# Optimization experiments

Hardware: AMD Instinct MI355X
Metric: run time of the kernel (lower is better)

Reference implementation:

```python
import jax, jax.numpy as jnp
import numpy as np

B, NV, NQ = 32, 512, 128
V_DIM, Q_DIM, H_DIM, K, H_OUT = 2048, 1024, 512, 3, 8
HK = H_DIM * K  # 1536


def setup_inputs() -> dict:
    key = jax.random.key(0)
    ks = jax.random.split(key, 8)
    s_v = 1.0 / np.sqrt(V_DIM)
    s_q = 1.0 / np.sqrt(Q_DIM)
    return {
        "v": jax.random.normal(ks[0], (B, NV, V_DIM), dtype=jnp.float32),
        "q": jax.random.normal(ks[1], (B, NQ, Q_DIM), dtype=jnp.float32),
        "Wv": jax.random.uniform(ks[2], (HK, V_DIM), jnp.float32, -s_v, s_v),
        "bv": jax.random.uniform(ks[3], (HK,), jnp.float32, -s_v, s_v),
        "Wq": jax.random.uniform(ks[4], (HK, Q_DIM), jnp.float32, -s_q, s_q),
        "bq": jax.random.uniform(ks[5], (HK,), jnp.float32, -s_q, s_q),
        "h_mat": jax.random.normal(ks[6], (H_OUT, HK), dtype=jnp.float32),
        "h_bias": jax.random.normal(ks[7], (H_OUT,), dtype=jnp.float32),
    }


def reference(v, q, Wv, bv, Wq, bq, h_mat, h_bias):
    # FCNet (single weight-norm Linear + ReLU); dropout is identity at eval.
    v_ = jax.nn.relu(jnp.einsum('bvd,kd->bvk', v, Wv) + bv)  # (B, NV, HK)
    q_ = jax.nn.relu(jnp.einsum('bqd,kd->bqk', q, Wq) + bq)  # (B, NQ, HK)
    # Three-way low-rank bilinear contraction over the rank dim k.
    logits = jnp.einsum('hk,bvk,bqk->bhvq', h_mat, v_, q_)
    return logits + h_bias[None, :, None, None]
```

## Files before the change

kernel.cpp:

```cpp
#include <hip/hip_runtime.h>


typedef _Float16 h8 __attribute__((ext_vector_type(8)));
typedef float f32x4 __attribute__((ext_vector_type(4)));

#define B_   32
#define NV_  512
#define NQ_  128
#define VD_  2048
#define QD_  1024
#define HK_  1536
#define HO_  8

__device__ __forceinline__ void gload_lds16(const void* g, void* l) {
  __builtin_amdgcn_global_load_lds(
      (const __attribute__((address_space(1))) void*)g,
      (__attribute__((address_space(3))) void*)l, 16, 0, 0);
}

__global__ __launch_bounds__(256) void cvt_all(
    const float* __restrict__ v, const float* __restrict__ q,
    const float* __restrict__ Wv, const float* __restrict__ Wq,
    const float* __restrict__ hm,
    _Float16* __restrict__ v16, _Float16* __restrict__ q16,
    _Float16* __restrict__ Wv16, _Float16* __restrict__ Wq16,
    _Float16* __restrict__ h16) {
  int i = blockIdx.x * blockDim.x + threadIdx.x;
  const float* src;
  _Float16* dst;
  if (i < 4194304)      { src = v;  dst = v16; }
  else if (i < 4718592) { src = q;  dst = q16;  i -= 4194304; }
  else if (i < 5111808) { src = Wv; dst = Wv16; i -= 4718592; }
  else if (i < 5308416) { src = Wq; dst = Wq16; i -= 5111808; }
  else                  { src = hm; dst = h16;  i -= 5308416; }
  const float4* p = (const float4*)src;
  float4 a = p[i * 2], b = p[i * 2 + 1];
  h8 o;
  o[0] = (_Float16)a.x; o[1] = (_Float16)a.y; o[2] = (_Float16)a.z; o[3] = (_Float16)a.w;
  o[4] = (_Float16)b.x; o[5] = (_Float16)b.y; o[6] = (_Float16)b.z; o[7] = (_Float16)b.w;
  ((h8*)dst)[i] = o;
}

template <int KTOT, bool REMAP>
__global__ __launch_bounds__(256, 3) void gemm_m97_relu_f16(
    const _Float16* __restrict__ A, const _Float16* __restrict__ Bw,
    const float* __restrict__ bias, _Float16* __restrict__ out, int N) {
  __shared__ __align__(16) _Float16 As[2][128 * 32];
  __shared__ __align__(16) _Float16 Bs[2][128 * 32];

  const int t = threadIdx.x;
  const int lane = t & 63;
  const int wave = t >> 6;
  const int wm = wave >> 1, wn = wave & 1;

  int bcol, brow;
  if (REMAP) {
    const int nwg = gridDim.x * gridDim.y;
    const int j = blockIdx.y * gridDim.x + blockIdx.x;
    const int l = (j & 7) * (nwg >> 3) + (j >> 3);
    bcol = (l % gridDim.x) * 128;
    brow = (l / gridDim.x) * 128;
  } else {
    bcol = blockIdx.x * 128;
    brow = blockIdx.y * 128;
  }

  const int scol = ((t & 3) ^ ((t >> 3) & 3)) * 8;
  const _Float16* Ab = A + (size_t)(brow + (t >> 2)) * KTOT + scol;
  const _Float16* Bb = Bw + (size_t)(bcol + (t >> 2)) * KTOT + scol;

  f32x4 acc[4][4] = {};

  for (int kt = 0; kt < KTOT / 64; ++kt) {
    __syncthreads();
#pragma unroll
    for (int kk = 0; kk < 2; ++kk) {
      gload_lds16(Ab + kt * 64 + kk * 32, &As[kk][t * 8]);
      gload_lds16(Ab + (size_t)64 * KTOT + kt * 64 + kk * 32, &As[kk][2048 + t * 8]);
      gload_lds16(Bb + kt * 64 + kk * 32, &Bs[kk][t * 8]);
      gload_lds16(Bb + (size_t)64 * KTOT + kt * 64 + kk * 32, &Bs[kk][2048 + t * 8]);
    }
    asm volatile("s_waitcnt vmcnt(0)" ::: "memory");
    __syncthreads();
#pragma unroll
    for (int kk = 0; kk < 2; ++kk) {
      h8 af[4], bf[4];
#pragma unroll
      for (int m = 0; m < 4; ++m) {
        const int row = wm * 64 + m * 16 + (lane & 15);
        af[m] = *(const h8*)&As[kk][row * 32 + ((lane >> 4) ^ ((row >> 1) & 3)) * 8];
      }
#pragma unroll
      for (int n = 0; n < 4; ++n) {
        const int row = wn * 64 + n * 16 + (lane & 15);
        bf[n] = *(const h8*)&Bs[kk][row * 32 + ((lane >> 4) ^ ((row >> 1) & 3)) * 8];
      }
#pragma unroll
      for (int m = 0; m < 4; ++m)
#pragma unroll
        for (int n = 0; n < 4; ++n)
          acc[m][n] = __builtin_amdgcn_mfma_f32_16x16x32_f16(af[m], bf[n], acc[m][n], 0, 0, 0);
    }
  }

#pragma unroll
  for (int m = 0; m < 4; ++m)
#pragma unroll
    for (int n = 0; n < 4; ++n) {
      const int col = bcol + wn * 64 + n * 16 + (lane & 15);
      const float bb = bias[col];
#pragma unroll
      for (int r = 0; r < 4; ++r) {
        const int row = brow + wm * 64 + m * 16 + (lane >> 4) * 4 + r;
        float val = acc[m][n][r] + bb;
        out[(size_t)row * N + col] = (_Float16)(val > 0.f ? val : 0.f);
      }
    }
}

template <int KTOT>
__global__ __launch_bounds__(256, 3) void gemm_m97_64_relu_f16(
    const _Float16* __restrict__ A, const _Float16* __restrict__ Bw,
    const float* __restrict__ bias, _Float16* __restrict__ out, int N) {
  __shared__ __align__(16) _Float16 As[2][64 * 32];
  __shared__ __align__(16) _Float16 Bs[2][128 * 32];

  const int t = threadIdx.x;
  const int lane = t & 63;
  const int wave = t >> 6;
  const int wm = wave >> 1, wn = wave & 1;
  const int bcol = blockIdx.x * 128;
  const int brow = blockIdx.y * 64;

  const int scol = ((t & 3) ^ ((t >> 3) & 3)) * 8;
  const _Float16* Ab = A + (size_t)(brow + (t >> 2)) * KTOT + scol;
  const _Float16* Bb = Bw + (size_t)(bcol + (t >> 2)) * KTOT + scol;

  f32x4 acc[2][4] = {};

  for (int kt = 0; kt < KTOT / 64; ++kt) {
    __syncthreads();
#pragma unroll
    for (int kk = 0; kk < 2; ++kk) {
      gload_lds16(Ab + kt * 64 + kk * 32, &As[kk][t * 8]);
      gload_lds16(Bb + kt * 64 + kk * 32, &Bs[kk][t * 8]);
      gload_lds16(Bb + (size_t)64 * KTOT + kt * 64 + kk * 32, &Bs[kk][2048 + t * 8]);
    }
    asm volatile("s_waitcnt vmcnt(0)" ::: "memory");
    __syncthreads();
#pragma unroll
    for (int kk = 0; kk < 2; ++kk) {
      h8 af[2], bf[4];
#pragma unroll
      for (int m = 0; m < 2; ++m) {
        const int row = wm * 32 + m * 16 + (lane & 15);
        af[m] = *(const h8*)&As[kk][row * 32 + ((lane >> 4) ^ ((row >> 1) & 3)) * 8];
      }
#pragma unroll
      for (int n = 0; n < 4; ++n) {
        const int row = wn * 64 + n * 16 + (lane & 15);
        bf[n] = *(const h8*)&Bs[kk][row * 32 + ((lane >> 4) ^ ((row >> 1) & 3)) * 8];
      }
#pragma unroll
      for (int m = 0; m < 2; ++m)
#pragma unroll
        for (int n = 0; n < 4; ++n)
          acc[m][n] = __builtin_amdgcn_mfma_f32_16x16x32_f16(af[m], bf[n], acc[m][n], 0, 0, 0);
    }
  }

#pragma unroll
  for (int m = 0; m < 2; ++m)
#pragma unroll
    for (int n = 0; n < 4; ++n) {
      const int col = bcol + wn * 64 + n * 16 + (lane & 15);
      const float bb = bias[col];
#pragma unroll
      for (int r = 0; r < 4; ++r) {
        const int row = brow + wm * 32 + m * 16 + (lane >> 4) * 4 + r;
        float val = acc[m][n][r] + bb;
        out[(size_t)row * N + col] = (_Float16)(val > 0.f ? val : 0.f);
      }
    }
}

__global__ __launch_bounds__(256, 3) void bilinear_m97_f16(
    const _Float16* __restrict__ vh, const _Float16* __restrict__ qh,
    const _Float16* __restrict__ h16, const float* __restrict__ hbias,
    float* __restrict__ out) {
  __shared__ __align__(16) _Float16 As[2][128 * 32];
  __shared__ __align__(16) _Float16 Bs[2][128 * 32];
  __shared__ __align__(16) _Float16 hl[HK_];

  const int t = threadIdx.x;
  const int lane = t & 63;
  const int wave = t >> 6;
  const int wm = wave >> 1, wn = wave & 1;
  const int mt = blockIdx.x;
  const int bh = blockIdx.y;
  const int b = bh >> 3, h = bh & 7;

  const int scol = ((t & 3) ^ ((t >> 3) & 3)) * 8;
  const _Float16* Ab = vh + ((size_t)b * NV_ + mt * 128 + (t >> 2)) * HK_ + scol;
  const _Float16* Qb = qh + (size_t)b * NQ_ * HK_;

  for (int i = t; i < HK_ / 8; i += 256)
    *(h8*)&hl[i * 8] = *(const h8*)&h16[(size_t)h * HK_ + i * 8];

  const int qrow = t >> 2;
  const int qs = t & 3;

  f32x4 acc[4][4] = {};

  for (int kt = 0; kt < HK_ / 64; ++kt) {
    __syncthreads();
#pragma unroll
    for (int kk = 0; kk < 2; ++kk) {
      gload_lds16(Ab + kt * 64 + kk * 32, &As[kk][t * 8]);
      gload_lds16(Ab + (size_t)64 * HK_ + kt * 64 + kk * 32, &As[kk][2048 + t * 8]);
    }
#pragma unroll
    for (int u = 0; u < 2; ++u) {
      const int row = u * 64 + qrow;
#pragma unroll
      for (int kk = 0; kk < 2; ++kk) {
        const int col = kt * 64 + kk * 32 + qs * 8;
        h8 qv = *(const h8*)&Qb[(size_t)row * HK_ + col];
        h8 hv = *(const h8*)&hl[col];
        *(h8*)&Bs[kk][row * 32 + (qs ^ ((row >> 1) & 3)) * 8] = qv * hv;
      }
    }
    asm volatile("s_waitcnt vmcnt(0)" ::: "memory");
    __syncthreads();
#pragma unroll
    for (int kk = 0; kk < 2; ++kk) {
      h8 af[4], bf[4];
#pragma unroll
      for (int m = 0; m < 4; ++m) {
        const int row = wm * 64 + m * 16 + (lane & 15);
        af[m] = *(const h8*)&As[kk][row * 32 + ((lane >> 4) ^ ((row >> 1) & 3)) * 8];
      }
#pragma unroll
      for (int n = 0; n < 4; ++n) {
        const int row = wn * 64 + n * 16 + (lane & 15);
        bf[n] = *(const h8*)&Bs[kk][row * 32 + ((lane >> 4) ^ ((row >> 1) & 3)) * 8];
      }
#pragma unroll
      for (int m = 0; m < 4; ++m)
#pragma unroll
        for (int n = 0; n < 4; ++n)
          acc[m][n] = __builtin_amdgcn_mfma_f32_16x16x32_f16(af[m], bf[n], acc[m][n], 0, 0, 0);
    }
  }

  const float bb = hbias[h];
  float* O = out + ((size_t)bh * NV_ + (size_t)mt * 128) * NQ_;
#pragma unroll
  for (int m = 0; m < 4; ++m)
#pragma unroll
    for (int n = 0; n < 4; ++n)
#pragma unroll
      for (int r = 0; r < 4; ++r) {
        const int row = wm * 64 + m * 16 + (lane >> 4) * 4 + r;
        const int col = wn * 64 + n * 16 + (lane & 15);
        O[(size_t)row * NQ_ + col] = acc[m][n][r] + bb;
      }
}

extern "C" void kernel_launch(void* const* d_in, const int* in_sizes, int n_in,
                              void* d_out, int out_size, void* d_ws,
                              size_t ws_size, hipStream_t stream) {
  const float* v = (const float*)d_in[0];
  const float* q = (const float*)d_in[1];
  const float* Wv = (const float*)d_in[2];
  const float* bv = (const float*)d_in[3];
  const float* Wq = (const float*)d_in[4];
  const float* bq = (const float*)d_in[5];
  const float* hmat = (const float*)d_in[6];
  const float* hbias = (const float*)d_in[7];

  if (ws_size < 147873792u) return;

  char* ws = (char*)d_ws;
  _Float16* v16 = (_Float16*)(ws);
  _Float16* q16 = (_Float16*)(ws + 67108864);
  _Float16* Wv16 = (_Float16*)(ws + 75497472);
  _Float16* Wq16 = (_Float16*)(ws + 81788928);
  _Float16* vh = (_Float16*)(ws + 84934656);
  _Float16* qh = (_Float16*)(ws + 135266304);
  _Float16* h16 = (_Float16*)(ws + 147849216);

  cvt_all<<<dim3(20742), 256, 0, stream>>>(v, q, Wv, Wq, hmat,
                                           v16, q16, Wv16, Wq16, h16);

  gemm_m97_relu_f16<VD_, true><<<dim3(HK_ / 128, 16384 / 128), 256, 0, stream>>>(
      v16, Wv16, bv, vh, HK_);
  gemm_m97_64_relu_f16<QD_><<<dim3(HK_ / 128, 4096 / 64), 256, 0, stream>>>(
      q16, Wq16, bq, qh, HK_);

  bilinear_m97_f16<<<dim3(NV_ / 128, B_ * HO_), 256, 0, stream>>>(
      vh, qh, h16, hbias, (float*)d_out);
}
```

Before: 236.9 us.

## Fuse fp32-to-fp16 activation conversion into GEMM A-tile loads

Drops the standalone conversion of v and q to fp16. The two projection GEMMs now read fp32 activations directly, convert them in registers with packed round-toward-zero conversion, and write the swizzled fp16 tile to LDS, while weights are still pre-converted. This removes a full read-write pass over the large activation tensors. In exchange, the A operand now goes through registers as synchronous loads instead of async global-to-LDS copies, and each GEMM tile re-reads fp32 A once per column block (12 times), which doubles the bytes of those reads.

Result: slower. 265.8 us (+12.2%).

```diff
diff --git a/kernel.cpp b/kernel.cpp
--- a/kernel.cpp
+++ b/kernel.cpp
@@ -2,6 +2,8 @@
 
 
 typedef _Float16 h8 __attribute__((ext_vector_type(8)));
+typedef _Float16 h4 __attribute__((ext_vector_type(4)));
+typedef __fp16 fp16x2 __attribute__((ext_vector_type(2)));
 typedef float f32x4 __attribute__((ext_vector_type(4)));
 
 #define B_   32
@@ -18,21 +20,32 @@
       (__attribute__((address_space(3))) void*)l, 16, 0, 0);
 }
 
-__global__ __launch_bounds__(256) void cvt_all(
-    const float* __restrict__ v, const float* __restrict__ q,
+__device__ __forceinline__ h4 cvt4(float4 a) {
+  struct P { fp16x2 lo, hi; } p;
+  p.lo = __builtin_amdgcn_cvt_pkrtz(a.x, a.y);
+  p.hi = __builtin_amdgcn_cvt_pkrtz(a.z, a.w);
+  return __builtin_bit_cast(h4, p);
+}
+
+__device__ __forceinline__ h8 cvt8(float4 a, float4 b) {
+  h4 lo = cvt4(a), hi = cvt4(b);
+  h8 o;
+  o[0] = lo[0]; o[1] = lo[1]; o[2] = lo[2]; o[3] = lo[3];
+  o[4] = hi[0]; o[5] = hi[1]; o[6] = hi[2]; o[7] = hi[3];
+  return o;
+}
+
+__global__ __launch_bounds__(256) void cvt_w(
     const float* __restrict__ Wv, const float* __restrict__ Wq,
     const float* __restrict__ hm,
-    _Float16* __restrict__ v16, _Float16* __restrict__ q16,
     _Float16* __restrict__ Wv16, _Float16* __restrict__ Wq16,
     _Float16* __restrict__ h16) {
   int i = blockIdx.x * blockDim.x + threadIdx.x;
   const float* src;
   _Float16* dst;
-  if (i < 4194304)      { src = v;  dst = v16; }
-  else if (i < 4718592) { src = q;  dst = q16;  i -= 4194304; }
-  else if (i < 5111808) { src = Wv; dst = Wv16; i -= 4718592; }
-  else if (i < 5308416) { src = Wq; dst = Wq16; i -= 5111808; }
-  else                  { src = hm; dst = h16;  i -= 5308416; }
+  if (i < 393216)      { src = Wv; dst = Wv16; }
+  else if (i < 589824) { src = Wq; dst = Wq16; i -= 393216; }
+  else                 { src = hm; dst = h16;  i -= 589824; }
   const float4* p = (const float4*)src;
   float4 a = p[i * 2], b = p[i * 2 + 1];
   h8 o;
@@ -42,8 +55,8 @@
 }
 
 template <int KTOT, bool REMAP>
-__global__ __launch_bounds__(256, 3) void gemm_m97_relu_f16(
-    const _Float16* __restrict__ A, const _Float16* __restrict__ Bw,
+__global__ __launch_bounds__(256, 3) void gemm_c_relu(
+    const float* __restrict__ A32, const _Float16* __restrict__ Bw,
     const float* __restrict__ bias, _Float16* __restrict__ out, int N) {
   __shared__ __align__(16) _Float16 As[2][128 * 32];
   __shared__ __align__(16) _Float16 Bs[2][128 * 32];
@@ -66,20 +79,39 @@
   }
 
   const int scol = ((t & 3) ^ ((t >> 3) & 3)) * 8;
-  const _Float16* Ab = A + (size_t)(brow + (t >> 2)) * KTOT + scol;
   const _Float16* Bb = Bw + (size_t)(bcol + (t >> 2)) * KTOT + scol;
 
+  const int arow = t >> 1;
+  const int ah = (t & 1) * 2;
+  const float* Ab = A32 + (size_t)(brow + arow) * KTOT;
+  const int aswz = (arow >> 1) & 3;
+
   f32x4 acc[4][4] = {};
 
   for (int kt = 0; kt < KTOT / 64; ++kt) {
     __syncthreads();
 #pragma unroll
     for (int kk = 0; kk < 2; ++kk) {
-      gload_lds16(Ab + kt * 64 + kk * 32, &As[kk][t * 8]);
-      gload_lds16(Ab + (size_t)64 * KTOT + kt * 64 + kk * 32, &As[kk][2048 + t * 8]);
       gload_lds16(Bb + kt * 64 + kk * 32, &Bs[kk][t * 8]);
       gload_lds16(Bb + (size_t)64 * KTOT + kt * 64 + kk * 32, &Bs[kk][2048 + t * 8]);
     }
+    float4 f[8];
+#pragma unroll
+    for (int kk = 0; kk < 2; ++kk)
+#pragma unroll
+      for (int si = 0; si < 2; ++si) {
+        const float* p = Ab + kt * 64 + kk * 32 + (ah + si) * 8;
+        f[(kk * 2 + si) * 2] = *(const float4*)p;
+        f[(kk * 2 + si) * 2 + 1] = *(const float4*)(p + 4);
+      }
+#pragma unroll
+    for (int kk = 0; kk < 2; ++kk)
+#pragma unroll
+      for (int si = 0; si < 2; ++si) {
+        const int phys = (ah + si) ^ aswz;
+        *(h8*)&As[kk][arow * 32 + phys * 8] =
+            cvt8(f[(kk * 2 + si) * 2], f[(kk * 2 + si) * 2 + 1]);
+      }
     asm volatile("s_waitcnt vmcnt(0)" ::: "memory");
     __syncthreads();
 #pragma unroll
@@ -119,8 +151,8 @@
 }
 
 template <int KTOT>
-__global__ __launch_bounds__(256, 3) void gemm_m97_64_relu_f16(
-    const _Float16* __restrict__ A, const _Float16* __restrict__ Bw,
+__global__ __launch_bounds__(256, 3) void gemm_d64_relu(
+    const float* __restrict__ A32, const _Float16* __restrict__ Bw,
     const float* __restrict__ bias, _Float16* __restrict__ out, int N) {
   __shared__ __align__(16) _Float16 As[2][64 * 32];
   __shared__ __align__(16) _Float16 Bs[2][128 * 32];
@@ -133,19 +165,32 @@
   const int brow = blockIdx.y * 64;
 
   const int scol = ((t & 3) ^ ((t >> 3) & 3)) * 8;
-  const _Float16* Ab = A + (size_t)(brow + (t >> 2)) * KTOT + scol;
   const _Float16* Bb = Bw + (size_t)(bcol + (t >> 2)) * KTOT + scol;
 
+  const int arow = t >> 2;
+  const int as = t & 3;
+  const float* Ab = A32 + (size_t)(brow + arow) * KTOT;
+  const int aphys = as ^ ((arow >> 1) & 3);
+
   f32x4 acc[2][4] = {};
 
   for (int kt = 0; kt < KTOT / 64; ++kt) {
     __syncthreads();
 #pragma unroll
     for (int kk = 0; kk < 2; ++kk) {
-      gload_lds16(Ab + kt * 64 + kk * 32, &As[kk][t * 8]);
       gload_lds16(Bb + kt * 64 + kk * 32, &Bs[kk][t * 8]);
       gload_lds16(Bb + (size_t)64 * KTOT + kt * 64 + kk * 32, &Bs[kk][2048 + t * 8]);
     }
+    float4 f[4];
+#pragma unroll
+    for (int kk = 0; kk < 2; ++kk) {
+      const float* p = Ab + kt * 64 + kk * 32 + as * 8;
+      f[kk * 2] = *(const float4*)p;
+      f[kk * 2 + 1] = *(const float4*)(p + 4);
+    }
+#pragma unroll
+    for (int kk = 0; kk < 2; ++kk)
+      *(h8*)&As[kk][arow * 32 + aphys * 8] = cvt8(f[kk * 2], f[kk * 2 + 1]);
     asm volatile("s_waitcnt vmcnt(0)" ::: "memory");
     __syncthreads();
 #pragma unroll
@@ -282,21 +327,18 @@
   if (ws_size < 147873792u) return;
 
   char* ws = (char*)d_ws;
-  _Float16* v16 = (_Float16*)(ws);
-  _Float16* q16 = (_Float16*)(ws + 67108864);
   _Float16* Wv16 = (_Float16*)(ws + 75497472);
   _Float16* Wq16 = (_Float16*)(ws + 81788928);
   _Float16* vh = (_Float16*)(ws + 84934656);
   _Float16* qh = (_Float16*)(ws + 135266304);
   _Float16* h16 = (_Float16*)(ws + 147849216);
 
-  cvt_all<<<dim3(20742), 256, 0, stream>>>(v, q, Wv, Wq, hmat,
-                                           v16, q16, Wv16, Wq16, h16);
-
-  gemm_m97_relu_f16<VD_, true><<<dim3(HK_ / 128, 16384 / 128), 256, 0, stream>>>(
-      v16, Wv16, bv, vh, HK_);
-  gemm_m97_64_relu_f16<QD_><<<dim3(HK_ / 128, 4096 / 64), 256, 0, stream>>>(
-      q16, Wq16, bq, qh, HK_);
+  cvt_w<<<dim3(2310), 256, 0, stream>>>(Wv, Wq, hmat, Wv16, Wq16, h16);
+
+  gemm_c_relu<VD_, true><<<dim3(HK_ / 128, 16384 / 128), 256, 0, stream>>>(
+      v, Wv16, bv, vh, HK_);
+  gemm_d64_relu<QD_><<<dim3(HK_ / 128, 4096 / 64), 256, 0, stream>>>(
+      q, Wq16, bq, qh, HK_);
 
   bilinear_m97_f16<<<dim3(NV_ / 128, B_ * HO_), 256, 0, stream>>>(
       vh, qh, h16, hbias, (float*)d_out);
```
